# Kernel tuning notes

Measured on AMD Instinct MI355X. Metric: run time of the kernel, lower is better.

Reference implementation:

```python
import jax, jax.numpy as jnp
import numpy as np

ENC_DIMS = [768, 2048, 1024, 512, 128]   # [in_dim] + layers + [e_dim]
DEC_DIMS = ENC_DIMS[::-1]
NUM_LEVELS = 4    # len(num_emb_list)
NUM_EXPERTS = 10
CODEBOOK_K = 256  # codes per level per expert
BETA = 0.001


def setup_inputs() -> dict:
    key = jax.random.key(0)
    B = 32768
    ks = jax.random.split(key, 16)
    inp = {}
    inp["x"] = jax.random.normal(ks[0], (B, ENC_DIMS[0]), dtype=jnp.float32)
    inp["labels"] = jax.random.randint(ks[1], (B,), 0, NUM_EXPERTS)
    i = 2
    for l in range(4):
        inp[f"enc_w{l}"] = jax.random.normal(ks[i], (ENC_DIMS[l], ENC_DIMS[l + 1]), dtype=jnp.float32) * 0.02
        inp[f"enc_b{l}"] = jnp.zeros((ENC_DIMS[l + 1],), dtype=jnp.float32)
        i += 1
    for l in range(4):
        inp[f"dec_w{l}"] = jax.random.normal(ks[i], (DEC_DIMS[l], DEC_DIMS[l + 1]), dtype=jnp.float32) * 0.02
        inp[f"dec_b{l}"] = jnp.zeros((DEC_DIMS[l + 1],), dtype=jnp.float32)
        i += 1
    # per-level, per-expert codebooks: [L, E, K, D]
    inp["cb"] = jax.random.normal(ks[i], (NUM_LEVELS, NUM_EXPERTS, CODEBOOK_K, ENC_DIMS[-1]), dtype=jnp.float32) * 0.02
    return inp


def _mlp(h, ws, bs):
    # Linear + ReLU between layers, no activation on the last layer (dropout=0, bn=False)
    n = len(ws)
    for i in range(n):
        h = h @ ws[i] + bs[i]
        if i < n - 1:
            h = jax.nn.relu(h)
    return h


def _residual_quantize(z, labels, cb):
    # z: [B, D]; labels: [B] expert ids; cb: [L, E, K, D]
    res = z
    qsum = jnp.zeros_like(z)
    loss = jnp.zeros((), dtype=z.dtype)
    idx_list = []
    for l in range(cb.shape[0]):  # small fixed loop over quantization levels
        cbl = cb[l]  # [E, K, D]
        # squared distances to each sample's expert codebook:
        # d[b,k] = ||res_b||^2 - 2 res_b . C[lab_b,k] + ||C[lab_b,k]||^2
        dots = jnp.einsum('bd,ekd->bek', res, cbl)                       # [B, E, K]
        dots = jnp.take_along_axis(dots, labels[:, None, None], axis=1)[:, 0]  # [B, K]
        cnorm = jnp.sum(cbl * cbl, axis=-1)[labels]                      # [B, K]
        d = jnp.sum(res * res, axis=-1, keepdims=True) - 2.0 * dots + cnorm
        idx = jnp.argmin(d, axis=-1)                                     # [B]
        q = cbl[labels, idx]                                             # [B, D] gather
        # codebook loss + beta * commitment loss
        loss = loss + jnp.mean((q - jax.lax.stop_gradient(res)) ** 2) \
                    + BETA * jnp.mean((jax.lax.stop_gradient(q) - res) ** 2)
        qsum = qsum + q
        res = res - q
        idx_list.append(idx)
    # straight-through estimator on the full quantized vector
    x_q = z + jax.lax.stop_gradient(qsum - z)
    indices = jnp.stack(idx_list, axis=1)  # [B, L]
    return x_q, loss, indices


def reference(x, labels,
              enc_w0, enc_b0, enc_w1, enc_b1, enc_w2, enc_b2, enc_w3, enc_b3,
              dec_w0, dec_b0, dec_w1, dec_b1, dec_w2, dec_b2, dec_w3, dec_b3,
              cb):
    enc_ws = [enc_w0, enc_w1, enc_w2, enc_w3]
    enc_bs = [enc_b0, enc_b1, enc_b2, enc_b3]
    dec_ws = [dec_w0, dec_w1, dec_w2, dec_w3]
    dec_bs = [dec_b0, dec_b1, dec_b2, dec_b3]
    z = _mlp(x, enc_ws, enc_bs)                      # encoder -> [B, e_dim]
    x_q, rq_loss, indices = _residual_quantize(z, labels, cb)
    out = _mlp(x_q, dec_ws, dec_bs)                  # decoder -> [B, in_dim]
    return out, rq_loss, indices, x_q
```

## Files before the change

kernel.cpp:

```cpp
#include <hip/hip_runtime.h>
#include <cstdint>
#include <cstddef>


typedef _Float16 half8  __attribute__((ext_vector_type(8)));
typedef short    short8 __attribute__((ext_vector_type(8)));
typedef float    f32x4  __attribute__((ext_vector_type(4)));

__device__ __forceinline__ uint16_t f32_to_bf16(float v) {
    uint32_t u = __float_as_uint(v);
    u += 0x7fff + ((u >> 16) & 1);
    return (uint16_t)(u >> 16);
}
__device__ __forceinline__ uint16_t f32_to_f16_bits(float v) {
    _Float16 h = (_Float16)v;
    return __builtin_bit_cast(uint16_t, h);
}
__device__ __forceinline__ void split16(float v, uint16_t& hb, uint16_t& lb) {
    hb = f32_to_f16_bits(v);
    float hf = (float)__builtin_bit_cast(_Float16, hb);
    lb = f32_to_f16_bits((v - hf) * 2048.0f);
}

__device__ __forceinline__ float wave_sum(float v) {
    #pragma unroll
    for (int off = 32; off > 0; off >>= 1)
        v += __shfl_xor(v, off, 64);
    return v;
}

#define GLOAD_LDS16(g, l)                                                      \
    __builtin_amdgcn_global_load_lds(                                          \
        (const __attribute__((address_space(1))) void*)(g),                    \
        (__attribute__((address_space(3))) void*)(l), 16, 0, 0)

__device__ __forceinline__ void wait_vm(int nf) {
    if (nf >= 12)     asm volatile("s_waitcnt vmcnt(12)" ::: "memory");
    else if (nf >= 8) asm volatile("s_waitcnt vmcnt(8)"  ::: "memory");
    else if (nf >= 6) asm volatile("s_waitcnt vmcnt(6)"  ::: "memory");
    else if (nf >= 4) asm volatile("s_waitcnt vmcnt(4)"  ::: "memory");
    else              asm volatile("s_waitcnt vmcnt(0)"  ::: "memory");
}
template<int N>
__device__ __forceinline__ void wait_vmK() {
    if constexpr (N == 3)      asm volatile("s_waitcnt vmcnt(3)" ::: "memory");
    else if constexpr (N == 6) asm volatile("s_waitcnt vmcnt(6)" ::: "memory");
    else                       asm volatile("s_waitcnt vmcnt(0)" ::: "memory");
}
__device__ __forceinline__ void wait_lg0() { asm volatile("s_waitcnt lgkmcnt(0)" ::: "memory"); }

template<bool F16> struct VecT        { using type = half8;  };
template<>         struct VecT<false> { using type = short8; };

__device__ __forceinline__ f32x4 mfma16(half8 a, half8 b, f32x4 c) {
    return __builtin_amdgcn_mfma_f32_16x16x32_f16(a, b, c, 0, 0, 0);
}
__device__ __forceinline__ f32x4 mfma16(short8 a, short8 b, f32x4 c) {
    return __builtin_amdgcn_mfma_f32_16x16x32_bf16(a, b, c, 0, 0, 0);
}

template<bool ISF16, bool CORR, bool RELU, int OUT>
__global__ __launch_bounds__(512, 2)
void gemm_256(const uint16_t* __restrict__ A, const uint16_t* __restrict__ Wt,
              const float* __restrict__ bias,
              float* __restrict__ Cf, uint16_t* __restrict__ C0,
              uint16_t* __restrict__ C1, int M, int K, int N) {
    using vec8 = typename VecT<ISF16>::type;
    constexpr int NPL    = CORR ? 2 : 1;
    constexpr int ABYT   = 8192;
    constexpr int BBYT   = 16384;
    constexpr int TILE_B = NPL * (ABYT + BBYT);
    constexpr int NBUF   = 3;
    constexpr int LPS    = CORR ? 6 : 3;
    __shared__ __align__(16) char lds[NBUF * TILE_B];

    const int t    = threadIdx.x;
    const int lane = t & 63, wave = t >> 6;
    const int wm = wave >> 2, wn = wave & 3;
    const int bm = blockIdx.y, bn = blockIdx.x;

    const size_t planeA = (size_t)M * K;
    const size_t planeB = (size_t)N * K;

    const int r = t >> 2;
    const int c = (t & 3) ^ ((r >> 1) & 3);
    const uint16_t* gA  = A  + (size_t)(bm * 128 + r) * K + c * 8;
    const uint16_t* gB0 = Wt + (size_t)(bn * 256 + r) * K + c * 8;
    const uint16_t* gB1 = Wt + (size_t)(bn * 256 + 128 + r) * K + c * 8;

    const int l15 = lane & 15, quad = lane >> 4;
    const int cpf = quad ^ ((l15 >> 1) & 3);
    const int aoff = ((wm * 64 + l15) * 4 + cpf) * 16;
    const int boff = ((wn * 64 + l15) * 4 + cpf) * 16;

    f32x4 accM[4][4], accC[4][4];
    #pragma unroll
    for (int mi = 0; mi < 4; ++mi)
        #pragma unroll
        for (int nj = 0; nj < 4; ++nj)
            #pragma unroll
            for (int rr = 0; rr < 4; ++rr) { accM[mi][nj][rr] = 0.f; if (CORR) accC[mi][nj][rr] = 0.f; }

    const int nt = K >> 5;

    auto stageA = [&](int ti, int bi) {
        char* b = (char*)lds + bi * TILE_B;
        const int kb = ti * 32;
        GLOAD_LDS16(gA + kb, b + t * 16);
        if (CORR) GLOAD_LDS16(gA + planeA + kb, b + ABYT + t * 16);
    };
    auto stageBh = [&](int ti, int bi) {
        char* b = (char*)lds + bi * TILE_B + NPL * ABYT;
        const int kb = ti * 32;
        GLOAD_LDS16(gB0 + kb, b + t * 16);
        GLOAD_LDS16(gB1 + kb, b + 8192 + t * 16);
    };
    auto stageBl = [&](int ti, int bi) {
        char* b = (char*)lds + bi * TILE_B + NPL * ABYT + BBYT;
        const int kb = ti * 32;
        GLOAD_LDS16(gB0 + planeB + kb, b + t * 16);
        GLOAD_LDS16(gB1 + planeB + kb, b + 8192 + t * 16);
    };

    stageA(0, 0); stageBh(0, 0); if (CORR) stageBl(0, 0);
    stageA(1, 1); stageBh(1, 1); if (CORR) stageBl(1, 1);
    wait_vmK<LPS>();
    __builtin_amdgcn_sched_barrier(0);
    __builtin_amdgcn_s_barrier();

    int cur = 0;
    for (int it = 0; it < nt; ++it) {
        char* bufc = (char*)lds + cur * TILE_B;
        const int nx = it + 2;
        const bool st = nx < nt;
        int bi = cur + 2; if (bi >= NBUF) bi -= NBUF;

        if (st) { stageA(nx, bi); stageBh(nx, bi); if (CORR) stageBl(nx, bi); }

        vec8 a0[4], b0[4];
        #pragma unroll
        for (int i = 0; i < 4; ++i) {
            a0[i] = *(const vec8*)(bufc + aoff + i * 1024);
            b0[i] = *(const vec8*)(bufc + NPL * ABYT + boff + i * 1024);
        }
        #pragma unroll
        for (int mi = 0; mi < 4; ++mi)
            #pragma unroll
            for (int nj = 0; nj < 4; ++nj)
                accM[mi][nj] = mfma16(a0[mi], b0[nj], accM[mi][nj]);

        if (CORR) {
            vec8 b1[4];
            #pragma unroll
            for (int i = 0; i < 4; ++i)
                b1[i] = *(const vec8*)(bufc + NPL * ABYT + BBYT + boff + i * 1024);
            #pragma unroll
            for (int mi = 0; mi < 4; ++mi)
                #pragma unroll
                for (int nj = 0; nj < 4; ++nj)
                    accC[mi][nj] = mfma16(a0[mi], b1[nj], accC[mi][nj]);
            vec8 a1[4];
            #pragma unroll
            for (int i = 0; i < 4; ++i)
                a1[i] = *(const vec8*)(bufc + ABYT + aoff + i * 1024);
            #pragma unroll
            for (int mi = 0; mi < 4; ++mi)
                #pragma unroll
                for (int nj = 0; nj < 4; ++nj)
                    accC[mi][nj] = mfma16(a1[mi], b0[nj], accC[mi][nj]);
        }

        wait_lg0();
        wait_vmK<LPS>();
        __builtin_amdgcn_sched_barrier(0);
        __builtin_amdgcn_s_barrier();
        __builtin_amdgcn_sched_barrier(0);

        cur = cur + 1; if (cur == NBUF) cur = 0;
    }

    if (CORR) {
        #pragma unroll
        for (int mi = 0; mi < 4; ++mi)
            #pragma unroll
            for (int nj = 0; nj < 4; ++nj)
                #pragma unroll
                for (int rr = 0; rr < 4; ++rr)
                    accM[mi][nj][rr] += accC[mi][nj][rr] * (1.0f / 2048.0f);
    }

    const int colb = bn * 256 + wn * 64 + l15;
    const int rowb = bm * 128 + wm * 64 + quad * 4;
    float bz[4];
    #pragma unroll
    for (int nj = 0; nj < 4; ++nj) bz[nj] = bias[colb + nj * 16];

    #pragma unroll
    for (int mi = 0; mi < 4; ++mi)
        #pragma unroll
        for (int nj = 0; nj < 4; ++nj)
            #pragma unroll
            for (int rr = 0; rr < 4; ++rr) {
                float v = accM[mi][nj][rr] + bz[nj];
                if (RELU) v = fmaxf(v, 0.f);
                const size_t o = (size_t)(rowb + mi * 16 + rr) * N + colb + nj * 16;
                if (OUT == 0) {
                    Cf[o] = v;
                } else if (OUT == 1) {
                    uint16_t hb, lb; split16(v, hb, lb);
                    C0[o] = hb; C1[o] = lb;
                } else {
                    C0[o] = f32_to_bf16(v);
                }
            }
}

template<int NPL, int NBUF, int BN, bool ISF16, bool CORR, bool RELU, int OUT>
__global__ __launch_bounds__(256)
void gemm_mfma(const uint16_t* __restrict__ A, const uint16_t* __restrict__ Wt,
               const float* __restrict__ bias,
               float* __restrict__ Cf, uint16_t* __restrict__ C0,
               uint16_t* __restrict__ C1, int M, int K, int N) {
    using vec8 = typename VecT<ISF16>::type;
    constexpr int APL    = 8192;
    constexpr int BPL    = BN * 64;
    constexpr int TILE_B = NPL * (APL + BPL);
    constexpr int BSHOT  = BN / 64;
    constexpr int NR     = BN / 32;
    constexpr int LPT    = NPL * (2 + BSHOT);
    __shared__ __align__(16) char lds[NBUF * TILE_B];

    const int t    = threadIdx.x;
    const int lane = t & 63, wave = t >> 6;
    const int wm = wave >> 1, wn = wave & 1;
    const int bm = blockIdx.y, bn = blockIdx.x;

    const size_t planeA = (size_t)M * K;
    const size_t planeB = (size_t)N * K;

    const int r0 = t >> 2,        c0 = (t & 3) ^ ((r0 >> 1) & 3);
    const int r1 = 64 + (t >> 2), c1 = (t & 3) ^ ((r1 >> 1) & 3);

    const uint16_t* gA0 = A + (size_t)(bm * 128 + r0) * K + c0 * 8;
    const uint16_t* gA1 = A + (size_t)(bm * 128 + r1) * K + c1 * 8;
    const uint16_t* gB[2];
    gB[0] = Wt + (size_t)(bn * BN + r0) * K + c0 * 8;
    if (BSHOT == 2) gB[1] = Wt + (size_t)(bn * BN + r1) * K + c1 * 8;

    const int wb = wave * 1024;
    const int l15 = lane & 15, quad = lane >> 4;
    const int cpf = quad ^ ((l15 >> 1) & 3);
    const int aoff = ((wm * 64 + l15) * 4 + cpf) * 16;
    const int boff = ((wn * (BN / 2) + l15) * 4 + cpf) * 16;

    f32x4 accM[4][NR], accC[4][NR];
    #pragma unroll
    for (int mi = 0; mi < 4; ++mi)
        #pragma unroll
        for (int nj = 0; nj < NR; ++nj)
            #pragma unroll
            for (int r = 0; r < 4; ++r) { accM[mi][nj][r] = 0.f; if (CORR) accC[mi][nj][r] = 0.f; }

    const int nt = K >> 5;

    auto stage = [&](int ti, int bi) {
        char* bA = (char*)lds + bi * TILE_B;
        char* bB = bA + NPL * APL;
        const int kb = ti * 32;
        #pragma unroll
        for (int p = 0; p < NPL; ++p) {
            GLOAD_LDS16(gA0 + (size_t)p * planeA + kb, bA + p * APL + wb);
            GLOAD_LDS16(gA1 + (size_t)p * planeA + kb, bA + p * APL + 4096 + wb);
            #pragma unroll
            for (int s = 0; s < BSHOT; ++s)
                GLOAD_LDS16(gB[s] + (size_t)p * planeB + kb, bB + p * BPL + s * 4096 + wb);
        }
    };

    #pragma unroll
    for (int i = 0; i < NBUF - 1; ++i) stage(i, i);

    int cur = 0;
    for (int it = 0; it < nt; ++it) {
        const int nx = it + NBUF - 1;
        if (nx < nt) {
            int bi = cur + NBUF - 1; if (bi >= NBUF) bi -= NBUF;
            stage(nx, bi);
        }
        const int rem = nt - 1 - it;
        const int nf  = (rem < NBUF - 1 ? rem : NBUF - 1) * LPT;
        wait_vm(nf);
        __builtin_amdgcn_sched_barrier(0);
        __builtin_amdgcn_s_barrier();
        __builtin_amdgcn_sched_barrier(0);

        char* bA = (char*)lds + cur * TILE_B;
        char* bB = bA + NPL * APL;

        vec8 a0[4], b0[NR];
        #pragma unroll
        for (int i = 0; i < 4; ++i)
            a0[i] = *(const vec8*)(bA + aoff + i * 1024);
        #pragma unroll
        for (int i = 0; i < NR; ++i)
            b0[i] = *(const vec8*)(bB + boff + i * 1024);
        #pragma unroll
        for (int mi = 0; mi < 4; ++mi)
            #pragma unroll
            for (int nj = 0; nj < NR; ++nj)
                accM[mi][nj] = mfma16(a0[mi], b0[nj], accM[mi][nj]);

        if (CORR) {
            vec8 b1[NR];
            #pragma unroll
            for (int i = 0; i < NR; ++i)
                b1[i] = *(const vec8*)(bB + BPL + boff + i * 1024);
            #pragma unroll
            for (int mi = 0; mi < 4; ++mi)
                #pragma unroll
                for (int nj = 0; nj < NR; ++nj)
                    accC[mi][nj] = mfma16(a0[mi], b1[nj], accC[mi][nj]);
            vec8 a1[4];
            #pragma unroll
            for (int i = 0; i < 4; ++i)
                a1[i] = *(const vec8*)(bA + APL + aoff + i * 1024);
            #pragma unroll
            for (int mi = 0; mi < 4; ++mi)
                #pragma unroll
                for (int nj = 0; nj < NR; ++nj)
                    accC[mi][nj] = mfma16(a1[mi], b0[nj], accC[mi][nj]);
        }

        wait_lg0();
        __builtin_amdgcn_sched_barrier(0);
        __builtin_amdgcn_s_barrier();
        __builtin_amdgcn_sched_barrier(0);

        cur = cur + 1; if (cur == NBUF) cur = 0;
    }

    if (CORR) {
        #pragma unroll
        for (int mi = 0; mi < 4; ++mi)
            #pragma unroll
            for (int nj = 0; nj < NR; ++nj)
                #pragma unroll
                for (int r = 0; r < 4; ++r)
                    accM[mi][nj][r] += accC[mi][nj][r] * (1.0f / 2048.0f);
    }

    const int colb = bn * BN + wn * (BN / 2) + l15;
    const int rowb = bm * 128 + wm * 64 + quad * 4;
    float bz[NR];
    #pragma unroll
    for (int nj = 0; nj < NR; ++nj) bz[nj] = bias[colb + nj * 16];

    #pragma unroll
    for (int mi = 0; mi < 4; ++mi)
        #pragma unroll
        for (int nj = 0; nj < NR; ++nj)
            #pragma unroll
            for (int r = 0; r < 4; ++r) {
                float v = accM[mi][nj][r] + bz[nj];
                if (RELU) v = fmaxf(v, 0.f);
                const size_t o = (size_t)(rowb + mi * 16 + r) * N + colb + nj * 16;
                if (OUT == 0) {
                    Cf[o] = v;
                } else if (OUT == 1) {
                    uint16_t hb, lb; split16(v, hb, lb);
                    C0[o] = hb; C1[o] = lb;
                } else {
                    C0[o] = f32_to_bf16(v);
                }
            }
}

template<int MODE>
__global__ __launch_bounds__(256)
void prep_w(const float* __restrict__ W, uint16_t* __restrict__ out, int K, int N) {
    __shared__ float tile[32][33];
    const int tx = threadIdx.x & 31, ty = threadIdx.x >> 5;
    const int n0 = blockIdx.x * 32, k0 = blockIdx.y * 32;
    #pragma unroll
    for (int i = 0; i < 4; ++i)
        tile[ty + i * 8][tx] = W[(size_t)(k0 + ty + i * 8) * N + n0 + tx];
    __syncthreads();
    #pragma unroll
    for (int i = 0; i < 4; ++i) {
        float v = tile[tx][ty + i * 8];
        size_t o = (size_t)(n0 + ty + i * 8) * K + k0 + tx;
        if (MODE == 0) {
            uint16_t hb, lb; split16(v, hb, lb);
            out[o] = hb;
            out[o + (size_t)N * K] = lb;
        } else {
            out[o] = f32_to_bf16(v);
        }
    }
}

__global__ __launch_bounds__(256)
void split_x(const float* __restrict__ x, uint16_t* __restrict__ hi,
             uint16_t* __restrict__ lo, int n4) {
    int i = blockIdx.x * 256 + threadIdx.x;
    const int stride = gridDim.x * 256;
    for (; i < n4; i += stride) {
        float4 v = ((const float4*)x)[i];
        ushort4 h, l;
        split16(v.x, h.x, l.x); split16(v.y, h.y, l.y);
        split16(v.z, h.z, l.z); split16(v.w, h.w, l.w);
        ((ushort4*)hi)[i] = h;
        ((ushort4*)lo)[i] = l;
    }
}

__global__ __launch_bounds__(256)
void prep_cb2(const float* __restrict__ cb, uint16_t* __restrict__ cbh,
              uint16_t* __restrict__ cbl, float* __restrict__ cnorm) {
    const int t = threadIdx.x, wave = t >> 6, lane = t & 63;
    const int row = blockIdx.x * 4 + wave;
    const float2 v = *(const float2*)(cb + (size_t)row * 128 + lane * 2);
    ushort2 h, l;
    split16(v.x, h.x, l.x); split16(v.y, h.y, l.y);
    *(ushort2*)(cbh + (size_t)row * 128 + lane * 2) = h;
    *(ushort2*)(cbl + (size_t)row * 128 + lane * 2) = l;
    const float s = wave_sum(v.x * v.x + v.y * v.y);
    if (lane == 0) cnorm[row] = s;
}

__global__ __launch_bounds__(256)
void hist_kernel(const int* __restrict__ labels, int* __restrict__ off,
                 int* __restrict__ cnt) {
    __shared__ int h[10];
    const int t = threadIdx.x;
    if (t < 10) h[t] = 0;
    __syncthreads();
    for (int i = t; i < 32768; i += 256) atomicAdd(&h[labels[i]], 1);
    __syncthreads();
    if (t == 0) {
        int a = 0;
        for (int e = 0; e < 10; ++e) { off[e] = a; a += h[e]; }
        off[10] = a;
    }
    if (t < 10) cnt[t] = 0;
}

__global__ __launch_bounds__(256)
void scatter_kernel(const int* __restrict__ labels, const int* __restrict__ off,
                    int* __restrict__ cnt, int* __restrict__ perm) {
    __shared__ int h[10], base[10];
    const int t = threadIdx.x;
    const int r = blockIdx.x * 256 + t;
    if (t < 10) h[t] = 0;
    __syncthreads();
    const int e = labels[r];
    const int lr = atomicAdd(&h[e], 1);
    __syncthreads();
    if (t < 10) base[t] = (h[t] > 0) ? atomicAdd(&cnt[t], h[t]) : 0;
    __syncthreads();
    perm[off[e] + base[e] + lr] = r;
}

__global__ __launch_bounds__(256)
void gather_kernel(const int* __restrict__ perm, const float* __restrict__ z,
                   float* __restrict__ resp, uint16_t* __restrict__ resph,
                   uint16_t* __restrict__ respl) {
    const int t = threadIdx.x, wave = t >> 6, lane = t & 63;
    const int p = blockIdx.x * 4 + wave;
    const int r = perm[p];
    const float2 v = *(const float2*)(z + (size_t)r * 128 + lane * 2);
    *(float2*)(resp + (size_t)p * 128 + lane * 2) = v;
    ushort2 h, l;
    split16(v.x, h.x, l.x); split16(v.y, h.y, l.y);
    *(ushort2*)(resph + (size_t)p * 128 + lane * 2) = h;
    *(ushort2*)(respl + (size_t)p * 128 + lane * 2) = l;
}

#define BETA_F 0.001f

template<bool LAST>
__global__ __launch_bounds__(256)
void rq_level(int l, const int* __restrict__ off, const int* __restrict__ perm,
              const float* __restrict__ cb, const uint16_t* __restrict__ cbh,
              const uint16_t* __restrict__ cbl, const float* __restrict__ cnorm,
              float* __restrict__ resp, uint16_t* __restrict__ resph,
              uint16_t* __restrict__ respl, const float* __restrict__ z,
              float* __restrict__ out_idx, float* __restrict__ out_xq,
              float* __restrict__ out_loss, uint16_t* __restrict__ xqbf) {
    __shared__ __align__(16) uint16_t Ah[2048], Al[2048];
    __shared__ __align__(16) uint16_t Bh[8192], Bl[8192];
    __shared__ float redv[64][4];
    __shared__ int   redk[64][4];
    __shared__ int   kwin[64];
    __shared__ float wl[4];
    __shared__ int   soff[11];

    const int t = threadIdx.x, lane = t & 63, wave = t >> 6;
    if (t < 11) soff[t] = off[t];
    __syncthreads();

    int e = -1, tile = 0, acc = 0;
    #pragma unroll
    for (int i = 0; i < 10; ++i) {
        const int nb = (soff[i + 1] - soff[i] + 63) >> 6;
        if ((int)blockIdx.x < acc + nb && e < 0) { e = i; tile = blockIdx.x - acc; }
        acc += nb;
    }
    if (e < 0) return;
    const int p0 = soff[e] + tile * 64;
    const int nrows = min(64, soff[e + 1] - p0);
    const int le = l * 10 + e;

    const int l15 = lane & 15, quad = lane >> 4;
    const int wn = wave;

    const int ar = t >> 2;
    const int ac = (t & 3) ^ ((ar >> 1) & 3);
    const int arp = p0 + ((ar < nrows) ? ar : 0);
    const uint16_t* gAh = resph + (size_t)arp * 128 + ac * 8;
    const uint16_t* gAl = respl + (size_t)arp * 128 + ac * 8;
    const uint16_t* cbh_b = cbh + (size_t)le * 256 * 128;
    const uint16_t* cbl_b = cbl + (size_t)le * 256 * 128;

    f32x4 accM[4][4], accC[4][4];
    #pragma unroll
    for (int mi = 0; mi < 4; ++mi)
        #pragma unroll
        for (int nj = 0; nj < 4; ++nj)
            #pragma unroll
            for (int r = 0; r < 4; ++r) { accM[mi][nj][r] = 0.f; accC[mi][nj][r] = 0.f; }

    const int cpf = quad ^ ((l15 >> 1) & 3);

    for (int kc = 0; kc < 4; ++kc) {
        const int kk = kc * 32;
        __syncthreads();
        GLOAD_LDS16(gAh + kk, (char*)Ah + t * 16);
        GLOAD_LDS16(gAl + kk, (char*)Al + t * 16);
        #pragma unroll
        for (int rnd = 0; rnd < 4; ++rnd) {
            const int j = rnd * 256 + t;
            const int br = j >> 2;
            const int bc = (j & 3) ^ ((br >> 1) & 3);
            GLOAD_LDS16(cbh_b + (size_t)br * 128 + kk + bc * 8, (char*)Bh + j * 16);
            GLOAD_LDS16(cbl_b + (size_t)br * 128 + kk + bc * 8, (char*)Bl + j * 16);
        }
        __syncthreads();

        half8 ah[4], bh[4];
        #pragma unroll
        for (int i = 0; i < 4; ++i) {
            ah[i] = *(const half8*)((char*)Ah + ((i * 16 + l15) * 4 + cpf) * 16);
            bh[i] = *(const half8*)((char*)Bh + ((wn * 64 + i * 16 + l15) * 4 + cpf) * 16);
        }
        #pragma unroll
        for (int mi = 0; mi < 4; ++mi)
            #pragma unroll
            for (int nj = 0; nj < 4; ++nj)
                accM[mi][nj] = mfma16(ah[mi], bh[nj], accM[mi][nj]);

        half8 bl4[4];
        #pragma unroll
        for (int i = 0; i < 4; ++i)
            bl4[i] = *(const half8*)((char*)Bl + ((wn * 64 + i * 16 + l15) * 4 + cpf) * 16);
        #pragma unroll
        for (int mi = 0; mi < 4; ++mi)
            #pragma unroll
            for (int nj = 0; nj < 4; ++nj)
                accC[mi][nj] = mfma16(ah[mi], bl4[nj], accC[mi][nj]);

        half8 al4[4];
        #pragma unroll
        for (int i = 0; i < 4; ++i)
            al4[i] = *(const half8*)((char*)Al + ((i * 16 + l15) * 4 + cpf) * 16);
        #pragma unroll
        for (int mi = 0; mi < 4; ++mi)
            #pragma unroll
            for (int nj = 0; nj < 4; ++nj)
                accC[mi][nj] = mfma16(al4[mi], bh[nj], accC[mi][nj]);
    }

    float cnv[4];
    #pragma unroll
    for (int nj = 0; nj < 4; ++nj)
        cnv[nj] = cnorm[le * 256 + wn * 64 + nj * 16 + l15];

    #pragma unroll
    for (int mi = 0; mi < 4; ++mi)
        #pragma unroll
        for (int r = 0; r < 4; ++r) {
            float bv = 1e30f; int bk = 0;
            #pragma unroll
            for (int nj = 0; nj < 4; ++nj) {
                const float d = cnv[nj] -
                    2.f * (accM[mi][nj][r] + accC[mi][nj][r] * (1.0f / 2048.0f));
                const int k = wn * 64 + nj * 16 + l15;
                if (d < bv || (d == bv && k < bk)) { bv = d; bk = k; }
            }
            #pragma unroll
            for (int o = 1; o < 16; o <<= 1) {
                const float ov = __shfl_xor(bv, o, 64);
                const int   ok = __shfl_xor(bk, o, 64);
                if (ov < bv || (ov == bv && ok < bk)) { bv = ov; bk = ok; }
            }
            const int row = mi * 16 + quad * 4 + r;
            if (l15 == 0) { redv[row][wn] = bv; redk[row][wn] = bk; }
        }
    __syncthreads();

    if (wave == 0) {
        const int row = lane;
        if (row < nrows) {
            float bv = redv[row][0]; int bk = redk[row][0];
            #pragma unroll
            for (int w = 1; w < 4; ++w) {
                const float ov = redv[row][w]; const int ok = redk[row][w];
                if (ov < bv || (ov == bv && ok < bk)) { bv = ov; bk = ok; }
            }
            kwin[row] = bk;
            out_idx[(size_t)perm[p0 + row] * 4 + l] = (float)bk;
        }
    }
    __syncthreads();

    float lossw = 0.f;
    for (int i = 0; i < 16; ++i) {
        const int row = wave * 16 + i;
        if (row < nrows) {
            const int p = p0 + row;
            const int k = kwin[row];
            const float2 q2 = *(const float2*)(cb + ((size_t)le * 256 + k) * 128 + lane * 2);
            float2 r2 = *(float2*)(resp + (size_t)p * 128 + lane * 2);
            const float n0 = r2.x - q2.x, n1 = r2.y - q2.y;
            *(float2*)(resp + (size_t)p * 128 + lane * 2) = make_float2(n0, n1);
            if (!LAST) {
                ushort2 h, lo;
                split16(n0, h.x, lo.x); split16(n1, h.y, lo.y);
                *(ushort2*)(resph + (size_t)p * 128 + lane * 2) = h;
                *(ushort2*)(respl + (size_t)p * 128 + lane * 2) = lo;
            }
            lossw += wave_sum(n0 * n0 + n1 * n1);
            if (LAST) {
                const int orig = perm[p];
                const float2 z2 = *(const float2*)(z + (size_t)orig * 128 + lane * 2);
                const float xq0 = z2.x - n0, xq1 = z2.y - n1;
                out_xq[(size_t)orig * 128 + lane * 2]     = xq0;
                out_xq[(size_t)orig * 128 + lane * 2 + 1] = xq1;
                ushort2 xb; xb.x = f32_to_bf16(xq0); xb.y = f32_to_bf16(xq1);
                *(ushort2*)(xqbf + (size_t)orig * 128 + lane * 2) = xb;
            }
        }
    }
    if (lane == 0) wl[wave] = lossw;
    __syncthreads();
    if (t == 0)
        atomicAdd(out_loss, (wl[0] + wl[1] + wl[2] + wl[3]) *
                            ((1.0f + BETA_F) / (32768.0f * 128.0f)));
}


extern "C" void kernel_launch(void* const* d_in, const int* in_sizes, int n_in,
                              void* d_out, int out_size, void* d_ws, size_t ws_size,
                              hipStream_t stream) {
    const float* x      = (const float*)d_in[0];
    const int*   labels = (const int*)d_in[1];
    const float* ew[4]  = {(const float*)d_in[2], (const float*)d_in[4],
                           (const float*)d_in[6], (const float*)d_in[8]};
    const float* eb[4]  = {(const float*)d_in[3], (const float*)d_in[5],
                           (const float*)d_in[7], (const float*)d_in[9]};
    const float* dw[4]  = {(const float*)d_in[10], (const float*)d_in[12],
                           (const float*)d_in[14], (const float*)d_in[16]};
    const float* db[4]  = {(const float*)d_in[11], (const float*)d_in[13],
                           (const float*)d_in[15], (const float*)d_in[17]};
    const float* cb     = (const float*)d_in[18];

    float* out = (float*)d_out;
    const size_t LOSS_OFF = 25165824;
    const size_t IDX_OFF  = 25165825;
    const size_t XQ_OFF   = 25296897;

    char* W = (char*)d_ws;
    size_t off_b = 0;
    auto alloc = [&](size_t bytes) { char* p = W + off_b; off_b += (bytes + 255) & ~(size_t)255; return p; };
    char*     region1 = alloc(134217728);
    char*     region2 = alloc(67108864);
    float*    z       = (float*)alloc(32768ull * 128 * 4);
    uint16_t* xqbf    = (uint16_t*)alloc(32768ull * 128 * 2);
    uint16_t* wtE0 = (uint16_t*)alloc(2ull *  768 * 2048 * 2);
    uint16_t* wtE1 = (uint16_t*)alloc(2ull * 2048 * 1024 * 2);
    uint16_t* wtE2 = (uint16_t*)alloc(2ull * 1024 *  512 * 2);
    uint16_t* wtE3 = (uint16_t*)alloc(2ull *  512 *  128 * 2);
    uint16_t* wtD0 = (uint16_t*)alloc(128ull  *  512 * 2);
    uint16_t* wtD1 = (uint16_t*)alloc(512ull  * 1024 * 2);
    uint16_t* wtD2 = (uint16_t*)alloc(1024ull * 2048 * 2);
    uint16_t* wtD3 = (uint16_t*)alloc(2048ull *  768 * 2);

    char* r1 = region1;
    float*    resp  = (float*)r1;                      r1 += 32768ull * 128 * 4;
    uint16_t* resph = (uint16_t*)r1;                   r1 += 32768ull * 128 * 2;
    uint16_t* respl = (uint16_t*)r1;                   r1 += 32768ull * 128 * 2;
    uint16_t* cbh   = (uint16_t*)r1;                   r1 += 4ull * 10 * 256 * 128 * 2;
    uint16_t* cbl   = (uint16_t*)r1;                   r1 += 4ull * 10 * 256 * 128 * 2;
    float*    cnorm = (float*)r1;                      r1 += 4ull * 10 * 256 * 4;
    int*      permv = (int*)r1;                        r1 += 32768ull * 4;
    int*      eoff  = (int*)r1;                        r1 += 16 * 4;
    int*      ecnt  = (int*)r1;                        r1 += 16 * 4;

    dim3 blk(256);
    dim3 blk512(512);

    prep_w<0><<<dim3(2048/32,  768/32), blk, 0, stream>>>(ew[0], wtE0,  768, 2048);
    prep_w<0><<<dim3(1024/32, 2048/32), blk, 0, stream>>>(ew[1], wtE1, 2048, 1024);
    prep_w<0><<<dim3( 512/32, 1024/32), blk, 0, stream>>>(ew[2], wtE2, 1024,  512);
    prep_w<0><<<dim3( 128/32,  512/32), blk, 0, stream>>>(ew[3], wtE3,  512,  128);
    prep_w<1><<<dim3( 512/32,  128/32), blk, 0, stream>>>(dw[0], wtD0,  128,  512);
    prep_w<1><<<dim3(1024/32,  512/32), blk, 0, stream>>>(dw[1], wtD1,  512, 1024);
    prep_w<1><<<dim3(2048/32, 1024/32), blk, 0, stream>>>(dw[2], wtD2, 1024, 2048);
    prep_w<1><<<dim3( 768/32, 2048/32), blk, 0, stream>>>(dw[3], wtD3, 2048,  768);

    const int MH = 16384;
    for (int half = 0; half < 2; ++half) {
        const float* xh = x + (size_t)half * MH * 768;
        uint16_t* xpl = (uint16_t*)region2;
        split_x<<<1024, blk, 0, stream>>>(xh, xpl, xpl + (size_t)MH * 768, MH * 768 / 4);

        uint16_t* h1 = (uint16_t*)region1;
        gemm_256<true, true, true, 1><<<dim3(8, 128), blk512, 0, stream>>>(
            xpl, wtE0, eb[0], nullptr, h1, h1 + (size_t)MH * 2048, MH, 768, 2048);

        uint16_t* h2 = (uint16_t*)region2;
        gemm_256<true, true, true, 1><<<dim3(4, 128), blk512, 0, stream>>>(
            h1, wtE1, eb[1], nullptr, h2, h2 + (size_t)MH * 1024, MH, 2048, 1024);

        uint16_t* h3 = (uint16_t*)region1;
        gemm_256<true, true, true, 1><<<dim3(2, 128), blk512, 0, stream>>>(
            h2, wtE2, eb[2], nullptr, h3, h3 + (size_t)MH * 512, MH, 1024, 512);

        gemm_mfma<2, 2, 64, true, true, false, 0><<<dim3(2, 128), blk, 0, stream>>>(
            h3, wtE3, eb[3], z + (size_t)half * MH * 128, nullptr, nullptr, MH, 512, 128);
    }

    prep_cb2<<<2560, blk, 0, stream>>>(cb, cbh, cbl, cnorm);
    hist_kernel<<<1, blk, 0, stream>>>(labels, eoff, ecnt);
    scatter_kernel<<<128, blk, 0, stream>>>(labels, eoff, ecnt, permv);
    gather_kernel<<<8192, blk, 0, stream>>>(permv, z, resp, resph, respl);
    hipMemsetAsync((char*)d_out + LOSS_OFF * 4, 0, 4, stream);

    rq_level<false><<<522, blk, 0, stream>>>(0, eoff, permv, cb, cbh, cbl, cnorm,
        resp, resph, respl, z, out + IDX_OFF, out + XQ_OFF, out + LOSS_OFF, xqbf);
    rq_level<false><<<522, blk, 0, stream>>>(1, eoff, permv, cb, cbh, cbl, cnorm,
        resp, resph, respl, z, out + IDX_OFF, out + XQ_OFF, out + LOSS_OFF, xqbf);
    rq_level<false><<<522, blk, 0, stream>>>(2, eoff, permv, cb, cbh, cbl, cnorm,
        resp, resph, respl, z, out + IDX_OFF, out + XQ_OFF, out + LOSS_OFF, xqbf);
    rq_level<true ><<<522, blk, 0, stream>>>(3, eoff, permv, cb, cbh, cbl, cnorm,
        resp, resph, respl, z, out + IDX_OFF, out + XQ_OFF, out + LOSS_OFF, xqbf);

    const int M = 32768;
    uint16_t* d0 = (uint16_t*)region1;
    uint16_t* d1 = (uint16_t*)region2;
    uint16_t* d2 = (uint16_t*)region1;
    gemm_mfma<1, 3, 128, false, false, true, 2><<<dim3(4, 256), blk, 0, stream>>>(
        xqbf, wtD0, db[0], nullptr, d0, nullptr, M, 128, 512);
    gemm_256<false, false, true, 2><<<dim3(4, 256), blk512, 0, stream>>>(
        d0, wtD1, db[1], nullptr, d1, nullptr, M, 512, 1024);
    gemm_256<false, false, true, 2><<<dim3(8, 256), blk512, 0, stream>>>(
        d1, wtD2, db[2], nullptr, d2, nullptr, M, 1024, 2048);
    gemm_256<false, false, false, 0><<<dim3(3, 256), blk512, 0, stream>>>(
        d2, wtD3, db[3], out, nullptr, nullptr, M, 2048, 768);
}
```

Measured before the change: 1.842 ms.

## Double-buffer LDS fragment reads in registers across GEMM k-iterations

Restructures the GEMM main loop into a two-step unrolled body. The next tile's A/B fragments are loaded from LDS into a second register set while the current tile's MFMAs and correction MFMAs run. The goal is to hide LDS read latency behind matrix math. In exchange it needs more registers, which can lower occupancy. It also relies on an even tile count. The next buffer is read after only a per-thread vmcnt wait and before the workgroup barrier, so data staged by other threads may not yet be visible.

```diff
diff --git a/kernel.cpp b/kernel.cpp
--- a/kernel.cpp
+++ b/kernel.cpp
@@ -128,55 +128,76 @@
     __builtin_amdgcn_sched_barrier(0);
     __builtin_amdgcn_s_barrier();
 
-    int cur = 0;
-    for (int it = 0; it < nt; ++it) {
+    vec8 a0A[4], b0A[4], a0B[4], b0B[4];
+    #pragma unroll
+    for (int i = 0; i < 4; ++i) {
+        a0A[i] = *(const vec8*)((char*)lds + aoff + i * 1024);
+        b0A[i] = *(const vec8*)((char*)lds + NPL * ABYT + boff + i * 1024);
+    }
+
+    auto step = [&](int it, int cur, vec8 (&a0c)[4], vec8 (&b0c)[4],
+                    vec8 (&a0n)[4], vec8 (&b0n)[4]) {
         char* bufc = (char*)lds + cur * TILE_B;
+        int nb_ = cur + 1; if (nb_ == NBUF) nb_ = 0;
+        char* bufn = (char*)lds + nb_ * TILE_B;
+        int bi = cur + 2; if (bi >= NBUF) bi -= NBUF;
         const int nx = it + 2;
         const bool st = nx < nt;
-        int bi = cur + 2; if (bi >= NBUF) bi -= NBUF;
+        const bool rd = it + 1 < nt;
 
         if (st) { stageA(nx, bi); stageBh(nx, bi); if (CORR) stageBl(nx, bi); }
 
-        vec8 a0[4], b0[4];
-        #pragma unroll
-        for (int i = 0; i < 4; ++i) {
-            a0[i] = *(const vec8*)(bufc + aoff + i * 1024);
-            b0[i] = *(const vec8*)(bufc + NPL * ABYT + boff + i * 1024);
-        }
+        vec8 b1c[4], a1c[4];
+        if (CORR) {
+            #pragma unroll
+            for (int i = 0; i < 4; ++i) {
+                b1c[i] = *(const vec8*)(bufc + NPL * ABYT + BBYT + boff + i * 1024);
+                a1c[i] = *(const vec8*)(bufc + ABYT + aoff + i * 1024);
+            }
+        }
+
         #pragma unroll
         for (int mi = 0; mi < 4; ++mi)
             #pragma unroll
             for (int nj = 0; nj < 4; ++nj)
-                accM[mi][nj] = mfma16(a0[mi], b0[nj], accM[mi][nj]);
+                accM[mi][nj] = mfma16(a0c[mi], b0c[nj], accM[mi][nj]);
+
+        if (rd) {
+            if (st) wait_vmK<LPS>(); else wait_vmK<0>();
+            #pragma unroll
+            for (int i = 0; i < 4; ++i) {
+                a0n[i] = *(const vec8*)(bufn + aoff + i * 1024);
+                b0n[i] = *(const vec8*)(bufn + NPL * ABYT + boff + i * 1024);
+            }
+        }
 
         if (CORR) {
-            vec8 b1[4];
-            #pragma unroll
-            for (int i = 0; i < 4; ++i)
-                b1[i] = *(const vec8*)(bufc + NPL * ABYT + BBYT + boff + i * 1024);
             #pragma unroll
             for (int mi = 0; mi < 4; ++mi)
                 #pragma unroll
                 for (int nj = 0; nj < 4; ++nj)
-                    accC[mi][nj] = mfma16(a0[mi], b1[nj], accC[mi][nj]);
-            vec8 a1[4];
-            #pragma unroll
-            for (int i = 0; i < 4; ++i)
-                a1[i] = *(const vec8*)(bufc + ABYT + aoff + i * 1024);
+                    accC[mi][nj] = mfma16(a0c[mi], b1c[nj], accC[mi][nj]);
             #pragma unroll
             for (int mi = 0; mi < 4; ++mi)
                 #pragma unroll
                 for (int nj = 0; nj < 4; ++nj)
-                    accC[mi][nj] = mfma16(a1[mi], b0[nj], accC[mi][nj]);
-        }
-
-        wait_lg0();
-        wait_vmK<LPS>();
-        __builtin_amdgcn_sched_barrier(0);
-        __builtin_amdgcn_s_barrier();
-        __builtin_amdgcn_sched_barrier(0);
-
-        cur = cur + 1; if (cur == NBUF) cur = 0;
+                    accC[mi][nj] = mfma16(a1c[mi], b0c[nj], accC[mi][nj]);
+        }
+
+        if (rd) {
+            wait_lg0();
+            __builtin_amdgcn_sched_barrier(0);
+            __builtin_amdgcn_s_barrier();
+            __builtin_amdgcn_sched_barrier(0);
+        }
+    };
+
+    int cur = 0;
+    for (int it = 0; it < nt; it += 2) {
+        step(it, cur, a0A, b0A, a0B, b0B);
+        int cur1 = cur + 1; if (cur1 == NBUF) cur1 = 0;
+        step(it + 1, cur1, a0B, b0B, a0A, b0A);
+        cur = cur1 + 1; if (cur == NBUF) cur = 0;
     }
 
     if (CORR) {
```

Measured after the change: 1.894 ms. 1.03x slower.
